# Kernel tuning notes

Measured on AMD Instinct MI355X. Metric: run time of the kernel, lower is better.

## Reference

```python
import jax, jax.numpy as jnp
import numpy as np

HEADS = 8
CH = 256
DH = CH // HEADS  # 32
NB = 128          # nb_features
EPS = 1e-4


def setup_inputs() -> dict:
    key = jax.random.key(0)
    ks = jax.random.split(key, 8)
    b, c, h, w = 4, CH, 96, 96
    s = 1.0 / np.sqrt(CH)  # typical linear init scale
    x = jax.random.normal(ks[0], (b, c, h, w), dtype=jnp.float32)
    wq = jax.random.normal(ks[1], (CH, CH), dtype=jnp.float32) * s
    wk = jax.random.normal(ks[2], (CH, CH), dtype=jnp.float32) * s
    wv = jax.random.normal(ks[3], (CH, CH), dtype=jnp.float32) * s
    wo = jax.random.normal(ks[4], (CH, CH), dtype=jnp.float32) * s
    bo = jnp.zeros((CH,), dtype=jnp.float32)
    # FAVOR+ gaussian orthogonal random projection (nb_features, dim_head)
    pm = np.random.default_rng(0)
    blocks = []
    for _ in range(NB // DH):
        qmat, _ = np.linalg.qr(pm.standard_normal((DH, DH)))
        blocks.append(qmat.T)
    proj = np.concatenate(blocks, axis=0)
    # scale rows to chi-distributed norms (scaling=0 default in performer_pytorch)
    norms = np.linalg.norm(pm.standard_normal((NB, DH)), axis=1, keepdims=True)
    proj_mat = jnp.asarray(proj * norms, dtype=jnp.float32)
    wp = jax.random.normal(ks[5], (CH, CH, 1, 1), dtype=jnp.float32) * s
    bp = jnp.zeros((CH,), dtype=jnp.float32)
    return {"x": x, "wq": wq, "wk": wk, "wv": wv, "wo": wo, "bo": bo,
            "proj_mat": proj_mat, "wp": wp, "bp": bp}


def softmax_kernel(data, proj, is_query):
    # data: (b, h, n, d); proj: (m, d). Performer FAVOR+ positive softmax features.
    data_normalizer = data.shape[-1] ** -0.25
    ratio = proj.shape[0] ** -0.5
    data_dash = jnp.einsum('bhnd,md->bhnm', data * data_normalizer, proj)
    diag = (jnp.sum(data * data, axis=-1) * 0.5 * (data_normalizer ** 2))[..., None]
    if is_query:
        m = jnp.max(data_dash, axis=-1, keepdims=True)
    else:
        m = jnp.max(data_dash, axis=(-1, -2), keepdims=True)
    return ratio * (jnp.exp(data_dash - diag - m) + EPS)


def reference(x, wq, wk, wv, wo, bo, proj_mat, wp, bp):
    b, c, h, w = x.shape
    n = h * w
    xf = x.reshape(b, c, n).transpose(0, 2, 1)  # (b, n, c)

    def split_heads(t):
        return t.reshape(b, n, HEADS, DH).transpose(0, 2, 1, 3)  # (b, h, n, d)

    q = split_heads(xf @ wq.T)
    k = split_heads(xf @ wk.T)
    v = split_heads(xf @ wv.T)

    qp = softmax_kernel(q, proj_mat, True)   # (b, h, n, m)
    kp = softmax_kernel(k, proj_mat, False)  # (b, h, n, m)

    # non-causal linear attention
    k_sum = jnp.sum(kp, axis=-2)                                   # (b, h, m)
    d_inv = 1.0 / jnp.einsum('bhnm,bhm->bhn', qp, k_sum)           # (b, h, n)
    ctx = jnp.einsum('bhnm,bhnd->bhmd', kp, v)                     # (b, h, m, d)
    out = jnp.einsum('bhnm,bhmd->bhnd', qp, ctx) * d_inv[..., None]

    out = out.transpose(0, 2, 1, 3).reshape(b, n, c)  # merge heads
    out = out @ wo.T + bo                              # to_out (attn_out_bias=True)
    out = out.transpose(0, 2, 1).reshape(b, c, h, w)
    # 1x1 conv projection
    out = jnp.einsum('bchw,oc->bohw', out, wp[:, :, 0, 0]) + bp[None, :, None, None]
    return out
```

## Files before the change

### kernel.cpp

```cpp
#include <hip/hip_runtime.h>

#define NTOT 9216
#define NORMC 0.42044820762685725f
#define RATIO 0.08838834764831845f
#define FEPS 1e-4f

typedef _Float16 h8 __attribute__((ext_vector_type(8)));
typedef _Float16 h4 __attribute__((ext_vector_type(4)));
typedef float f4 __attribute__((ext_vector_type(4)));

__device__ __forceinline__ void gld16(const _Float16* g, _Float16* l) {
  __builtin_amdgcn_global_load_lds((const __attribute__((address_space(1))) void*)g,
                                   (__attribute__((address_space(3))) void*)l, 16, 0, 0);
}

__global__ __launch_bounds__(256) void prep_small(
    const float* __restrict__ wq, const float* __restrict__ wk,
    const float* __restrict__ wv, const float* __restrict__ proj,
    const float* __restrict__ wo, const float* __restrict__ bo,
    const float* __restrict__ wp, const float* __restrict__ bp,
    _Float16* __restrict__ Wall, _Float16* __restrict__ projh,
    _Float16* __restrict__ Wc, float* __restrict__ bc) {
  int r = blockIdx.x, t = threadIdx.x;
  if (r < 768) {
    const float* src = (r < 256) ? wq + (size_t)r * 256
                     : (r < 512) ? wk + (size_t)(r - 256) * 256
                                 : wv + (size_t)(r - 512) * 256;
    Wall[(size_t)r * 256 + t] = (_Float16)src[t];
  } else if (r < 784) {
    int idx = (r - 768) * 256 + t;
    projh[idx] = (_Float16)proj[idx];
  } else {
    int o = r - 784;
    float acc = 0.f;
    for (int c = 0; c < 256; ++c) acc += wp[o * 256 + c] * wo[c * 256 + t];
    Wc[o * 256 + t] = (_Float16)acc;
    if (t == 0) {
      float ab = bp[o];
      for (int c = 0; c < 256; ++c) ab += wp[o * 256 + c] * bo[c];
      bc[o] = ab;
    }
  }
}

__global__ __launch_bounds__(256) void prep_xT(
    const float* __restrict__ x, _Float16* __restrict__ xT) {
  __shared__ float T_s[64][65];
  int n0 = blockIdx.x * 64, c0 = blockIdx.y * 64, b = blockIdx.z;
  int t = threadIdx.x;
  for (int i = 0; i < 4; ++i) {
    int f = t + i * 256;
    int cc = f >> 4, n4 = f & 15;
    float4 a = *(const float4*)(x + ((size_t)(b * 256 + c0 + cc)) * NTOT + n0 + n4 * 4);
    T_s[cc][n4 * 4 + 0] = a.x;
    T_s[cc][n4 * 4 + 1] = a.y;
    T_s[cc][n4 * 4 + 2] = a.z;
    T_s[cc][n4 * 4 + 3] = a.w;
  }
  __syncthreads();
  for (int i = 0; i < 2; ++i) {
    int f = t + i * 256;
    int nn = f >> 3, c8 = f & 7;
    h8 hv;
    for (int j = 0; j < 8; ++j) hv[j] = (_Float16)T_s[c8 * 8 + j][nn];
    *(h8*)(xT + ((size_t)(b * NTOT + n0 + nn)) * 256 + c0 + c8 * 8) = hv;
  }
}

__global__ __launch_bounds__(256) void qkv_mfma(
    const _Float16* __restrict__ xT, const _Float16* __restrict__ Wall,
    _Float16* __restrict__ q, _Float16* __restrict__ k, _Float16* __restrict__ v) {
  __shared__ __align__(16) _Float16 A_s[128 * 32];
  __shared__ __align__(16) _Float16 B_s[128 * 32];
  int n0 = blockIdx.x * 128, co0 = blockIdx.y * 128, sel = blockIdx.z;
  _Float16* Out = (sel == 0) ? q : (sel == 1) ? k : v;
  const _Float16* Wb = Wall + (size_t)sel * 65536;
  int t = threadIdx.x, wave = t >> 6, lane = t & 63;
  int lm = lane & 15, lg = lane >> 4;
  int wm = (wave & 1) * 64, wn = (wave >> 1) * 64;
  int srow = wave * 32 + (lane >> 2);
  int scol = ((lane & 3) ^ ((lane >> 3) & 3)) * 8;
  const _Float16* gA = Wb + (size_t)(co0 + srow) * 256 + scol;
  const _Float16* gB = xT + (size_t)(n0 + srow) * 256 + scol;
  _Float16* lA = A_s + wave * 1024;
  _Float16* lB = B_s + wave * 1024;
  int pg = (lg ^ ((lm >> 1) & 3)) * 8;
  f4 acc[4][4] = {};
  for (int kt = 0; kt < 8; ++kt) {
    int c0 = kt * 32;
    __syncthreads();
    gld16(gA + c0, lA);
    gld16(gA + c0 + 16 * 256, lA + 512);
    gld16(gB + c0, lB);
    gld16(gB + c0 + 16 * 256, lB + 512);
    __syncthreads();
    h8 a[4], bf[4];
#pragma unroll
    for (int mi = 0; mi < 4; ++mi) a[mi] = *(const h8*)&A_s[(wm + mi * 16 + lm) * 32 + pg];
#pragma unroll
    for (int ni = 0; ni < 4; ++ni) bf[ni] = *(const h8*)&B_s[(wn + ni * 16 + lm) * 32 + pg];
#pragma unroll
    for (int mi = 0; mi < 4; ++mi)
#pragma unroll
      for (int ni = 0; ni < 4; ++ni)
        acc[mi][ni] = __builtin_amdgcn_mfma_f32_16x16x32_f16(a[mi], bf[ni], acc[mi][ni], 0, 0, 0);
  }
#pragma unroll
  for (int mi = 0; mi < 4; ++mi)
#pragma unroll
    for (int ni = 0; ni < 4; ++ni) {
      h4 hv;
#pragma unroll
      for (int r = 0; r < 4; ++r) hv[r] = (_Float16)acc[mi][ni][r];
      *(h4*)(Out + (size_t)(n0 + wn + ni * 16 + lm) * 256 + co0 + wm + mi * 16 + lg * 4) = hv;
    }
}

__global__ __launch_bounds__(256) void prep_vT(
    const _Float16* __restrict__ v, _Float16* __restrict__ vT) {
  __shared__ _Float16 T[64 * 132];
  int n0 = blockIdx.x * 128, c0 = blockIdx.y * 64, b = blockIdx.z;
  int t = threadIdx.x;
  for (int i = 0; i < 4; ++i) {
    int f = t + i * 256;
    int nl = f >> 3, cg = f & 7;
    h8 vv = *(const h8*)(v + ((size_t)(b * NTOT + n0 + nl)) * 256 + c0 + cg * 8);
#pragma unroll
    for (int j = 0; j < 8; ++j) T[(cg * 8 + j) * 132 + nl] = vv[j];
  }
  __syncthreads();
  int cl = t >> 2, seg = t & 3;
  _Float16* gout = vT + ((size_t)(b * 256 + c0 + cl)) * NTOT + n0 + seg * 32;
#pragma unroll
  for (int j = 0; j < 8; ++j)
    *(h4*)(gout + j * 4) = *(const h4*)&T[cl * 132 + seg * 32 + j * 4];
}

__global__ __launch_bounds__(256) void kmax_mfma(
    const _Float16* __restrict__ k, const _Float16* __restrict__ projh,
    float* __restrict__ kmaxp) {
  __shared__ __align__(16) _Float16 k_s[128 * 32];
  __shared__ float red4[4];
  int bh = blockIdx.y, b = bh >> 3, h = bh & 7;
  int nbase = blockIdx.x * 256;
  int t = threadIdx.x, wave = t >> 6, lane = t & 63, lm = lane & 15, lg = lane >> 4;
  h8 pr[8];
#pragma unroll
  for (int mt = 0; mt < 8; ++mt) pr[mt] = *(const h8*)&projh[(mt * 16 + lm) * 32 + lg * 8];
  int scol = ((lane & 3) ^ ((lane >> 3) & 3)) * 8;
  const _Float16* gK =
      k + ((size_t)(b * NTOT + nbase + wave * 32 + (lane >> 2))) * 256 + h * 32 + scol;
  _Float16* lK = k_s + wave * 1024;
  int pg = (lg ^ ((lm >> 1) & 3)) * 8;
  float vmax = -1e30f;
  for (int ch = 0; ch < 2; ++ch) {
    __syncthreads();
    gld16(gK + (size_t)(ch * 128) * 256, lK);
    gld16(gK + (size_t)(ch * 128) * 256 + 16 * 256, lK + 512);
    __syncthreads();
#pragma unroll
    for (int nt = 0; nt < 2; ++nt) {
      h8 a = *(const h8*)&k_s[(wave * 32 + nt * 16 + lm) * 32 + pg];
#pragma unroll
      for (int mt = 0; mt < 8; ++mt) {
        f4 z = {0.f, 0.f, 0.f, 0.f};
        f4 d = __builtin_amdgcn_mfma_f32_16x16x32_f16(a, pr[mt], z, 0, 0, 0);
        vmax = fmaxf(vmax, fmaxf(fmaxf(d[0], d[1]), fmaxf(d[2], d[3])));
      }
    }
  }
  for (int i = 1; i < 64; i <<= 1) vmax = fmaxf(vmax, __shfl_xor(vmax, i, 64));
  if (lane == 0) red4[wave] = vmax;
  __syncthreads();
  if (t == 0)
    kmaxp[bh * 36 + blockIdx.x] =
        NORMC * fmaxf(fmaxf(red4[0], red4[1]), fmaxf(red4[2], red4[3]));
}

__global__ __launch_bounds__(256) void ctx_mfma(
    const _Float16* __restrict__ k, const _Float16* __restrict__ vT,
    const _Float16* __restrict__ projh, const float* __restrict__ kmaxp,
    float* __restrict__ part) {
  __shared__ __align__(16) _Float16 k_s[128 * 32];
  __shared__ __align__(16) _Float16 vT_s[32 * 136];
  __shared__ __align__(16) _Float16 kpT[128 * 136];
  __shared__ float diag_s[128];
  __shared__ float kmax_sh;
  int bh = blockIdx.y, b = bh >> 3, h = bh & 7;
  int nbase = blockIdx.x * 384;
  int t = threadIdx.x, wave = t >> 6, lane = t & 63, lm = lane & 15, lg = lane >> 4;
  h8 pr[8];
#pragma unroll
  for (int mt = 0; mt < 8; ++mt) pr[mt] = *(const h8*)&projh[(mt * 16 + lm) * 32 + lg * 8];
  if (t == 0) {
    float mx = -1e30f;
    for (int i = 0; i < 36; ++i) mx = fmaxf(mx, kmaxp[bh * 36 + i]);
    kmax_sh = mx;
  }
  __syncthreads();
  float kmax = kmax_sh;
  int scol = ((lane & 3) ^ ((lane >> 3) & 3)) * 8;
  const _Float16* gK =
      k + ((size_t)(b * NTOT + nbase + wave * 32 + (lane >> 2))) * 256 + h * 32 + scol;
  const _Float16* gV = vT + ((size_t)(b * 256 + h * 32 + (t >> 3))) * NTOT + nbase;
  _Float16* lK = k_s + wave * 1024;
  int pg = (lg ^ ((lm >> 1) & 3)) * 8;
  f4 cacc[2][2] = {};
  float ks[8] = {};
  for (int ch = 0; ch < 3; ++ch) {
    gld16(gK + (size_t)(ch * 128) * 256, lK);
    gld16(gK + (size_t)(ch * 128) * 256 + 16 * 256, lK + 512);
    {
      int d = t >> 3, g = t & 7;
#pragma unroll
      for (int i = 0; i < 2; ++i) {
        h8 vv = *(const h8*)(gV + ch * 128 + (i * 8 + g) * 8);
        *(h8*)&vT_s[d * 136 + (i * 8 + g) * 8] = vv;
      }
    }
    __syncthreads();
    if (t < 128) {
      float s = 0.f;
#pragma unroll
      for (int c = 0; c < 4; ++c) {
        h8 kv = *(const h8*)&k_s[t * 32 + c * 8];
#pragma unroll
        for (int j = 0; j < 8; ++j) s += (float)kv[j] * (float)kv[j];
      }
      diag_s[t] = s * (0.5f * NORMC * NORMC);
    }
    f4 dsh[2][8];
#pragma unroll
    for (int nt = 0; nt < 2; ++nt) {
      h8 a = *(const h8*)&k_s[(wave * 32 + nt * 16 + lm) * 32 + pg];
#pragma unroll
      for (int mt = 0; mt < 8; ++mt) {
        f4 z = {0.f, 0.f, 0.f, 0.f};
        dsh[nt][mt] = __builtin_amdgcn_mfma_f32_16x16x32_f16(a, pr[mt], z, 0, 0, 0);
      }
    }
    __syncthreads();
#pragma unroll
    for (int nt = 0; nt < 2; ++nt)
#pragma unroll
      for (int mt = 0; mt < 8; ++mt) {
        h4 hv;
        float lsum = 0.f;
#pragma unroll
        for (int r = 0; r < 4; ++r) {
          int nl = wave * 32 + nt * 16 + lg * 4 + r;
          float val = RATIO * (__expf(NORMC * dsh[nt][mt][r] - diag_s[nl] - kmax) + FEPS);
          hv[r] = (_Float16)val;
          lsum += val;
        }
        ks[mt] += lsum;
        *(h4*)&kpT[(mt * 16 + lm) * 136 + wave * 32 + nt * 16 + lg * 4] = hv;
      }
    __syncthreads();
#pragma unroll
    for (int k2 = 0; k2 < 4; ++k2) {
      h8 a2[2], b2[2];
#pragma unroll
      for (int mt2 = 0; mt2 < 2; ++mt2)
        a2[mt2] = *(const h8*)&kpT[(wave * 32 + mt2 * 16 + lm) * 136 + k2 * 32 + lg * 8];
#pragma unroll
      for (int dt = 0; dt < 2; ++dt)
        b2[dt] = *(const h8*)&vT_s[(dt * 16 + lm) * 136 + k2 * 32 + lg * 8];
#pragma unroll
      for (int mt2 = 0; mt2 < 2; ++mt2)
#pragma unroll
        for (int dt = 0; dt < 2; ++dt)
          cacc[mt2][dt] =
              __builtin_amdgcn_mfma_f32_16x16x32_f16(a2[mt2], b2[dt], cacc[mt2][dt], 0, 0, 0);
    }
    __syncthreads();
  }
  float* pp = part + (size_t)(blockIdx.y * 24 + blockIdx.x) * 4224;
#pragma unroll
  for (int mt2 = 0; mt2 < 2; ++mt2)
#pragma unroll
    for (int dt = 0; dt < 2; ++dt)
      *(f4*)(pp + (dt * 16 + lm) * 128 + wave * 32 + mt2 * 16 + lg * 4) = cacc[mt2][dt];
  float* redk = (float*)kpT;
#pragma unroll
  for (int mt = 0; mt < 8; ++mt) {
    float s = ks[mt];
    s += __shfl_xor(s, 16, 64);
    s += __shfl_xor(s, 32, 64);
    if (lg == 0) redk[wave * 128 + mt * 16 + lm] = s;
  }
  __syncthreads();
  if (t < 128)
    pp[32 * 128 + t] = redk[t] + redk[128 + t] + redk[256 + t] + redk[384 + t];
}

__global__ __launch_bounds__(256) void reduce_ctx(
    const float* __restrict__ part, float* __restrict__ ctx_aug) {
  int bh = blockIdx.x, t = threadIdx.x;
  const float* pb = part + (size_t)bh * 24 * 4224;
  for (int it = 0; it < 17; ++it) {
    int cell = t + it * 256;
    if (cell < 4224) {
      float s = 0.f;
      for (int p = 0; p < 24; ++p) s += pb[(size_t)p * 4224 + cell];
      int d = cell >> 7, m = cell & 127;
      ctx_aug[(size_t)bh * 4608 + m * 36 + d] = s;
    }
  }
}

__global__ __launch_bounds__(256) void attn_mfma(
    const _Float16* __restrict__ q, const _Float16* __restrict__ projh,
    const float* __restrict__ ctx_aug, _Float16* __restrict__ attn) {
  __shared__ __align__(16) _Float16 q_sh[128 * 32];
  __shared__ __align__(16) _Float16 qp_s[128 * 136];
  __shared__ __align__(16) _Float16 ctxT[32 * 136];
  __shared__ float ksum_s[128];
  int n0 = blockIdx.x * 128;
  int bh = blockIdx.y, b = bh >> 3, h = bh & 7;
  int t = threadIdx.x, wave = t >> 6, lane = t & 63, lm = lane & 15, lg = lane >> 4;
  const float* cb = ctx_aug + (size_t)bh * 4608;
  h8 pr[8];
#pragma unroll
  for (int mt = 0; mt < 8; ++mt) pr[mt] = *(const h8*)&projh[(mt * 16 + lm) * 32 + lg * 8];
  int scol = ((lane & 3) ^ ((lane >> 3) & 3)) * 8;
  const _Float16* gQ =
      q + ((size_t)(b * NTOT + n0 + wave * 32 + (lane >> 2))) * 256 + h * 32 + scol;
  gld16(gQ, q_sh + wave * 1024);
  gld16(gQ + 16 * 256, q_sh + wave * 1024 + 512);
  {
    int m = t >> 1, dbase = (t & 1) * 16;
#pragma unroll
    for (int g = 0; g < 4; ++g) {
      float4 cv = *(const float4*)(cb + m * 36 + dbase + g * 4);
      ctxT[(dbase + g * 4 + 0) * 136 + m] = (_Float16)cv.x;
      ctxT[(dbase + g * 4 + 1) * 136 + m] = (_Float16)cv.y;
      ctxT[(dbase + g * 4 + 2) * 136 + m] = (_Float16)cv.z;
      ctxT[(dbase + g * 4 + 3) * 136 + m] = (_Float16)cv.w;
    }
  }
  if (t < 128) ksum_s[t] = cb[t * 36 + 32];
  __syncthreads();
  int pg = (lg ^ ((lm >> 1) & 3)) * 8;
  float diag_r[2];
#pragma unroll
  for (int nt = 0; nt < 2; ++nt) {
    int n = wave * 32 + nt * 16 + lm;
    float s = 0.f;
#pragma unroll
    for (int c = 0; c < 4; ++c) {
      h8 qv = *(const h8*)&q_sh[n * 32 + c * 8];
#pragma unroll
      for (int j = 0; j < 8; ++j) s += (float)qv[j] * (float)qv[j];
    }
    diag_r[nt] = s * (0.5f * NORMC * NORMC);
  }
  f4 dsh[2][8];
#pragma unroll
  for (int nt = 0; nt < 2; ++nt) {
    h8 qf = *(const h8*)&q_sh[(wave * 32 + nt * 16 + lm) * 32 + pg];
#pragma unroll
    for (int mt = 0; mt < 8; ++mt) {
      f4 z = {0.f, 0.f, 0.f, 0.f};
      dsh[nt][mt] = __builtin_amdgcn_mfma_f32_16x16x32_f16(pr[mt], qf, z, 0, 0, 0);
    }
  }
  float den_r[2];
#pragma unroll
  for (int nt = 0; nt < 2; ++nt) {
    float mx = -1e30f;
#pragma unroll
    for (int mt = 0; mt < 8; ++mt)
#pragma unroll
      for (int r = 0; r < 4; ++r) mx = fmaxf(mx, dsh[nt][mt][r]);
    mx = fmaxf(mx, __shfl_xor(mx, 16, 64));
    mx = fmaxf(mx, __shfl_xor(mx, 32, 64));
    float den = 0.f;
#pragma unroll
    for (int mt = 0; mt < 8; ++mt) {
      h4 hv;
#pragma unroll
      for (int r = 0; r < 4; ++r) {
        float val = RATIO * (__expf(NORMC * (dsh[nt][mt][r] - mx) - diag_r[nt]) + FEPS);
        hv[r] = (_Float16)val;
        den += val * ksum_s[mt * 16 + lg * 4 + r];
      }
      *(h4*)&qp_s[(wave * 32 + nt * 16 + lm) * 136 + mt * 16 + lg * 4] = hv;
    }
    den += __shfl_xor(den, 16, 64);
    den += __shfl_xor(den, 32, 64);
    den_r[nt] = 1.f / den;
  }
  __syncthreads();
  f4 oacc[2][2] = {};
#pragma unroll
  for (int k2 = 0; k2 < 4; ++k2) {
    h8 ac[2], bq[2];
#pragma unroll
    for (int dt = 0; dt < 2; ++dt)
      ac[dt] = *(const h8*)&ctxT[(dt * 16 + lm) * 136 + k2 * 32 + lg * 8];
#pragma unroll
    for (int nt = 0; nt < 2; ++nt)
      bq[nt] = *(const h8*)&qp_s[(wave * 32 + nt * 16 + lm) * 136 + k2 * 32 + lg * 8];
#pragma unroll
    for (int dt = 0; dt < 2; ++dt)
#pragma unroll
      for (int nt = 0; nt < 2; ++nt)
        oacc[dt][nt] = __builtin_amdgcn_mfma_f32_16x16x32_f16(ac[dt], bq[nt], oacc[dt][nt], 0, 0, 0);
  }
#pragma unroll
  for (int dt = 0; dt < 2; ++dt)
#pragma unroll
    for (int nt = 0; nt < 2; ++nt) {
      int n = wave * 32 + nt * 16 + lm;
      h4 hv;
#pragma unroll
      for (int r = 0; r < 4; ++r) hv[r] = (_Float16)(oacc[dt][nt][r] * den_r[nt]);
      *(h4*)(attn + ((size_t)(b * NTOT + n0 + n)) * 256 + h * 32 + dt * 16 + lg * 4) = hv;
    }
}

__global__ __launch_bounds__(256) void out_mfma(
    const _Float16* __restrict__ Wc, const _Float16* __restrict__ attn,
    const float* __restrict__ bc, float* __restrict__ out) {
  __shared__ __align__(16) _Float16 A_s[128 * 32];
  __shared__ __align__(16) _Float16 B_s[128 * 32];
  int bx = blockIdx.x;
  int o0 = blockIdx.y * 128;
  int b = bx / 72, nb0 = (bx % 72) * 128;
  int t = threadIdx.x, wave = t >> 6, lane = t & 63;
  int lm = lane & 15, lg = lane >> 4;
  int wm = (wave & 1) * 64, wn = (wave >> 1) * 64;
  int srow = wave * 32 + (lane >> 2);
  int scol = ((lane & 3) ^ ((lane >> 3) & 3)) * 8;
  const _Float16* gA = Wc + (size_t)(o0 + srow) * 256 + scol;
  const _Float16* gB = attn + (size_t)(b * NTOT + nb0 + srow) * 256 + scol;
  _Float16* lA = A_s + wave * 1024;
  _Float16* lB = B_s + wave * 1024;
  int pg = (lg ^ ((lm >> 1) & 3)) * 8;
  f4 acc[4][4] = {};
  for (int kt = 0; kt < 8; ++kt) {
    int c0 = kt * 32;
    __syncthreads();
    gld16(gA + c0, lA);
    gld16(gA + c0 + 16 * 256, lA + 512);
    gld16(gB + c0, lB);
    gld16(gB + c0 + 16 * 256, lB + 512);
    __syncthreads();
    h8 a[4], bf[4];
#pragma unroll
    for (int mi = 0; mi < 4; ++mi) a[mi] = *(const h8*)&A_s[(wm + mi * 16 + lm) * 32 + pg];
#pragma unroll
    for (int ni = 0; ni < 4; ++ni) bf[ni] = *(const h8*)&B_s[(wn + ni * 16 + lm) * 32 + pg];
#pragma unroll
    for (int mi = 0; mi < 4; ++mi)
#pragma unroll
      for (int ni = 0; ni < 4; ++ni)
        acc[mi][ni] = __builtin_amdgcn_mfma_f32_16x16x32_f16(bf[ni], a[mi], acc[mi][ni], 0, 0, 0);
  }
#pragma unroll
  for (int mi = 0; mi < 4; ++mi) {
    int o = o0 + wm + mi * 16 + lm;
    float bias = bc[o];
#pragma unroll
    for (int ni = 0; ni < 4; ++ni) {
      f4 ov = acc[mi][ni];
      float4 st = make_float4(ov[0] + bias, ov[1] + bias, ov[2] + bias, ov[3] + bias);
      *(float4*)(out + ((size_t)(b * 256 + o)) * NTOT + nb0 + wn + ni * 16 + lg * 4) = st;
    }
  }
}

extern "C" void kernel_launch(void* const* d_in, const int* in_sizes, int n_in,
                              void* d_out, int out_size, void* d_ws, size_t ws_size,
                              hipStream_t stream) {
  const float* x = (const float*)d_in[0];
  const float* wq = (const float*)d_in[1];
  const float* wk = (const float*)d_in[2];
  const float* wv = (const float*)d_in[3];
  const float* wo = (const float*)d_in[4];
  const float* bo = (const float*)d_in[5];
  const float* proj = (const float*)d_in[6];
  const float* wp = (const float*)d_in[7];
  const float* bp = (const float*)d_in[8];
  float* out = (float*)d_out;
  float* ws = (float*)d_ws;

  float* part = ws;
  float* ctx_aug = part + 3244032;
  float* kmaxp = ctx_aug + 147456;
  float* bc = kmaxp + 1152;
  _Float16* hb = (_Float16*)(bc + 256);
  const size_t THALF = (size_t)4 * NTOT * 256;
  _Float16* q_h = hb;
  _Float16* k_h = q_h + THALF;
  _Float16* v_h = k_h + THALF;
  _Float16* xT = v_h + THALF;
  _Float16* vTg = xT + THALF;
  _Float16* Wall = vTg + THALF;
  _Float16* Wc = Wall + 768 * 256;
  _Float16* projh = Wc + 65536;

  prep_small<<<1040, 256, 0, stream>>>(wq, wk, wv, proj, wo, bo, wp, bp, Wall, projh, Wc, bc);
  prep_xT<<<dim3(144, 4, 4), 256, 0, stream>>>(x, xT);
  qkv_mfma<<<dim3(288, 2, 3), 256, 0, stream>>>(xT, Wall, q_h, k_h, v_h);
  prep_vT<<<dim3(72, 4, 4), 256, 0, stream>>>(v_h, vTg);
  kmax_mfma<<<dim3(36, 32), 256, 0, stream>>>(k_h, projh, kmaxp);
  ctx_mfma<<<dim3(24, 32), 256, 0, stream>>>(k_h, vTg, projh, kmaxp, part);
  reduce_ctx<<<32, 256, 0, stream>>>(part, ctx_aug);
  attn_mfma<<<dim3(72, 32), 256, 0, stream>>>(q_h, projh, ctx_aug, xT);
  out_mfma<<<dim3(288, 2), 256, 0, stream>>>(Wc, xT, bc, out);
}
```

Measured before the change: 252.2 us.

## Fuse prep kernels, fold vT transpose and key max into QKV GEMM

Merges prep_small and prep_xT into one launch. The QKV GEMM now writes V directly in transposed layout by swapping the MFMA operands, and it computes the per-tile key-feature max from the K tile held in shared memory, which removes the separate prep_vT and kmax kernels and one full pass over K and V. reduce_ctx is split across four times as many blocks and emits fp16 ctxT plus ksum directly, so attn_mfma loads ctx straight into registers instead of transposing it in shared memory. The cost is extra shared memory and epilogue work in the QKV kernel, with only the K blocks doing the max pass.

```diff
diff --git a/kernel.cpp b/kernel.cpp
--- a/kernel.cpp
+++ b/kernel.cpp
@@ -14,24 +14,50 @@
                                    (__attribute__((address_space(3))) void*)l, 16, 0, 0);
 }
 
-__global__ __launch_bounds__(256) void prep_small(
-    const float* __restrict__ wq, const float* __restrict__ wk,
-    const float* __restrict__ wv, const float* __restrict__ proj,
-    const float* __restrict__ wo, const float* __restrict__ bo,
-    const float* __restrict__ wp, const float* __restrict__ bp,
+__global__ __launch_bounds__(256) void prep(
+    const float* __restrict__ x, const float* __restrict__ wq,
+    const float* __restrict__ wk, const float* __restrict__ wv,
+    const float* __restrict__ proj, const float* __restrict__ wo,
+    const float* __restrict__ bo, const float* __restrict__ wp,
+    const float* __restrict__ bp, _Float16* __restrict__ xT,
     _Float16* __restrict__ Wall, _Float16* __restrict__ projh,
     _Float16* __restrict__ Wc, float* __restrict__ bc) {
+  __shared__ float T_s[64][65];
   int r = blockIdx.x, t = threadIdx.x;
-  if (r < 768) {
-    const float* src = (r < 256) ? wq + (size_t)r * 256
-                     : (r < 512) ? wk + (size_t)(r - 256) * 256
-                                 : wv + (size_t)(r - 512) * 256;
-    Wall[(size_t)r * 256 + t] = (_Float16)src[t];
-  } else if (r < 784) {
-    int idx = (r - 768) * 256 + t;
+  if (r < 2304) {
+    int nx = r % 144, rem = r / 144;
+    int cy = rem & 3, b = rem >> 2;
+    int n0 = nx * 64, c0 = cy * 64;
+    for (int i = 0; i < 4; ++i) {
+      int f = t + i * 256;
+      int cc = f >> 4, n4 = f & 15;
+      float4 a = *(const float4*)(x + ((size_t)(b * 256 + c0 + cc)) * NTOT + n0 + n4 * 4);
+      T_s[cc][n4 * 4 + 0] = a.x;
+      T_s[cc][n4 * 4 + 1] = a.y;
+      T_s[cc][n4 * 4 + 2] = a.z;
+      T_s[cc][n4 * 4 + 3] = a.w;
+    }
+    __syncthreads();
+    for (int i = 0; i < 2; ++i) {
+      int f = t + i * 256;
+      int nn = f >> 3, c8 = f & 7;
+      h8 hv;
+      for (int j = 0; j < 8; ++j) hv[j] = (_Float16)T_s[c8 * 8 + j][nn];
+      *(h8*)(xT + ((size_t)(b * NTOT + n0 + nn)) * 256 + c0 + c8 * 8) = hv;
+    }
+    return;
+  }
+  int r2 = r - 2304;
+  if (r2 < 768) {
+    const float* src = (r2 < 256) ? wq + (size_t)r2 * 256
+                     : (r2 < 512) ? wk + (size_t)(r2 - 256) * 256
+                                  : wv + (size_t)(r2 - 512) * 256;
+    Wall[(size_t)r2 * 256 + t] = (_Float16)src[t];
+  } else if (r2 < 784) {
+    int idx = (r2 - 768) * 256 + t;
     projh[idx] = (_Float16)proj[idx];
   } else {
-    int o = r - 784;
+    int o = r2 - 784;
     float acc = 0.f;
     for (int c = 0; c < 256; ++c) acc += wp[o * 256 + c] * wo[c * 256 + t];
     Wc[o * 256 + t] = (_Float16)acc;
@@ -43,37 +69,17 @@
   }
 }
 
-__global__ __launch_bounds__(256) void prep_xT(
-    const float* __restrict__ x, _Float16* __restrict__ xT) {
-  __shared__ float T_s[64][65];
-  int n0 = blockIdx.x * 64, c0 = blockIdx.y * 64, b = blockIdx.z;
-  int t = threadIdx.x;
-  for (int i = 0; i < 4; ++i) {
-    int f = t + i * 256;
-    int cc = f >> 4, n4 = f & 15;
-    float4 a = *(const float4*)(x + ((size_t)(b * 256 + c0 + cc)) * NTOT + n0 + n4 * 4);
-    T_s[cc][n4 * 4 + 0] = a.x;
-    T_s[cc][n4 * 4 + 1] = a.y;
-    T_s[cc][n4 * 4 + 2] = a.z;
-    T_s[cc][n4 * 4 + 3] = a.w;
-  }
-  __syncthreads();
-  for (int i = 0; i < 2; ++i) {
-    int f = t + i * 256;
-    int nn = f >> 3, c8 = f & 7;
-    h8 hv;
-    for (int j = 0; j < 8; ++j) hv[j] = (_Float16)T_s[c8 * 8 + j][nn];
-    *(h8*)(xT + ((size_t)(b * NTOT + n0 + nn)) * 256 + c0 + c8 * 8) = hv;
-  }
-}
-
 __global__ __launch_bounds__(256) void qkv_mfma(
     const _Float16* __restrict__ xT, const _Float16* __restrict__ Wall,
-    _Float16* __restrict__ q, _Float16* __restrict__ k, _Float16* __restrict__ v) {
+    const _Float16* __restrict__ projh, _Float16* __restrict__ q,
+    _Float16* __restrict__ k, _Float16* __restrict__ vT,
+    float* __restrict__ kmaxp) {
   __shared__ __align__(16) _Float16 A_s[128 * 32];
   __shared__ __align__(16) _Float16 B_s[128 * 32];
-  int n0 = blockIdx.x * 128, co0 = blockIdx.y * 128, sel = blockIdx.z;
-  _Float16* Out = (sel == 0) ? q : (sel == 1) ? k : v;
+  __shared__ __align__(16) _Float16 ktile[64 * 132];
+  int bx = blockIdx.x, co0 = blockIdx.y * 128, sel = blockIdx.z;
+  int b = bx / 72, ntile = bx % 72;
+  int n0 = bx * 128;
   const _Float16* Wb = Wall + (size_t)sel * 65536;
   int t = threadIdx.x, wave = t >> 6, lane = t & 63;
   int lm = lane & 15, lg = lane >> 4;
@@ -86,95 +92,104 @@
   _Float16* lB = B_s + wave * 1024;
   int pg = (lg ^ ((lm >> 1) & 3)) * 8;
   f4 acc[4][4] = {};
-  for (int kt = 0; kt < 8; ++kt) {
-    int c0 = kt * 32;
-    __syncthreads();
-    gld16(gA + c0, lA);
-    gld16(gA + c0 + 16 * 256, lA + 512);
-    gld16(gB + c0, lB);
-    gld16(gB + c0 + 16 * 256, lB + 512);
-    __syncthreads();
-    h8 a[4], bf[4];
-#pragma unroll
-    for (int mi = 0; mi < 4; ++mi) a[mi] = *(const h8*)&A_s[(wm + mi * 16 + lm) * 32 + pg];
-#pragma unroll
-    for (int ni = 0; ni < 4; ++ni) bf[ni] = *(const h8*)&B_s[(wn + ni * 16 + lm) * 32 + pg];
+  if (sel < 2) {
+    for (int kt = 0; kt < 8; ++kt) {
+      int c0 = kt * 32;
+      __syncthreads();
+      gld16(gA + c0, lA);
+      gld16(gA + c0 + 16 * 256, lA + 512);
+      gld16(gB + c0, lB);
+      gld16(gB + c0 + 16 * 256, lB + 512);
+      __syncthreads();
+      h8 a[4], bf[4];
+#pragma unroll
+      for (int mi = 0; mi < 4; ++mi) a[mi] = *(const h8*)&A_s[(wm + mi * 16 + lm) * 32 + pg];
+#pragma unroll
+      for (int ni = 0; ni < 4; ++ni) bf[ni] = *(const h8*)&B_s[(wn + ni * 16 + lm) * 32 + pg];
+#pragma unroll
+      for (int mi = 0; mi < 4; ++mi)
+#pragma unroll
+        for (int ni = 0; ni < 4; ++ni)
+          acc[mi][ni] = __builtin_amdgcn_mfma_f32_16x16x32_f16(a[mi], bf[ni], acc[mi][ni], 0, 0, 0);
+    }
+    _Float16* Out = (sel == 0) ? q : k;
 #pragma unroll
     for (int mi = 0; mi < 4; ++mi)
 #pragma unroll
-      for (int ni = 0; ni < 4; ++ni)
-        acc[mi][ni] = __builtin_amdgcn_mfma_f32_16x16x32_f16(a[mi], bf[ni], acc[mi][ni], 0, 0, 0);
-  }
-#pragma unroll
-  for (int mi = 0; mi < 4; ++mi)
-#pragma unroll
-    for (int ni = 0; ni < 4; ++ni) {
-      h4 hv;
-#pragma unroll
-      for (int r = 0; r < 4; ++r) hv[r] = (_Float16)acc[mi][ni][r];
-      *(h4*)(Out + (size_t)(n0 + wn + ni * 16 + lm) * 256 + co0 + wm + mi * 16 + lg * 4) = hv;
-    }
-}
-
-__global__ __launch_bounds__(256) void prep_vT(
-    const _Float16* __restrict__ v, _Float16* __restrict__ vT) {
-  __shared__ _Float16 T[64 * 132];
-  int n0 = blockIdx.x * 128, c0 = blockIdx.y * 64, b = blockIdx.z;
-  int t = threadIdx.x;
-  for (int i = 0; i < 4; ++i) {
-    int f = t + i * 256;
-    int nl = f >> 3, cg = f & 7;
-    h8 vv = *(const h8*)(v + ((size_t)(b * NTOT + n0 + nl)) * 256 + c0 + cg * 8);
-#pragma unroll
-    for (int j = 0; j < 8; ++j) T[(cg * 8 + j) * 132 + nl] = vv[j];
-  }
-  __syncthreads();
-  int cl = t >> 2, seg = t & 3;
-  _Float16* gout = vT + ((size_t)(b * 256 + c0 + cl)) * NTOT + n0 + seg * 32;
-#pragma unroll
-  for (int j = 0; j < 8; ++j)
-    *(h4*)(gout + j * 4) = *(const h4*)&T[cl * 132 + seg * 32 + j * 4];
-}
-
-__global__ __launch_bounds__(256) void kmax_mfma(
-    const _Float16* __restrict__ k, const _Float16* __restrict__ projh,
-    float* __restrict__ kmaxp) {
-  __shared__ __align__(16) _Float16 k_s[128 * 32];
-  __shared__ float red4[4];
-  int bh = blockIdx.y, b = bh >> 3, h = bh & 7;
-  int nbase = blockIdx.x * 256;
-  int t = threadIdx.x, wave = t >> 6, lane = t & 63, lm = lane & 15, lg = lane >> 4;
-  h8 pr[8];
-#pragma unroll
-  for (int mt = 0; mt < 8; ++mt) pr[mt] = *(const h8*)&projh[(mt * 16 + lm) * 32 + lg * 8];
-  int scol = ((lane & 3) ^ ((lane >> 3) & 3)) * 8;
-  const _Float16* gK =
-      k + ((size_t)(b * NTOT + nbase + wave * 32 + (lane >> 2))) * 256 + h * 32 + scol;
-  _Float16* lK = k_s + wave * 1024;
-  int pg = (lg ^ ((lm >> 1) & 3)) * 8;
-  float vmax = -1e30f;
-  for (int ch = 0; ch < 2; ++ch) {
-    __syncthreads();
-    gld16(gK + (size_t)(ch * 128) * 256, lK);
-    gld16(gK + (size_t)(ch * 128) * 256 + 16 * 256, lK + 512);
-    __syncthreads();
-#pragma unroll
-    for (int nt = 0; nt < 2; ++nt) {
-      h8 a = *(const h8*)&k_s[(wave * 32 + nt * 16 + lm) * 32 + pg];
-#pragma unroll
-      for (int mt = 0; mt < 8; ++mt) {
-        f4 z = {0.f, 0.f, 0.f, 0.f};
-        f4 d = __builtin_amdgcn_mfma_f32_16x16x32_f16(a, pr[mt], z, 0, 0, 0);
-        vmax = fmaxf(vmax, fmaxf(fmaxf(d[0], d[1]), fmaxf(d[2], d[3])));
-      }
-    }
-  }
-  for (int i = 1; i < 64; i <<= 1) vmax = fmaxf(vmax, __shfl_xor(vmax, i, 64));
-  if (lane == 0) red4[wave] = vmax;
-  __syncthreads();
-  if (t == 0)
-    kmaxp[bh * 36 + blockIdx.x] =
-        NORMC * fmaxf(fmaxf(red4[0], red4[1]), fmaxf(red4[2], red4[3]));
+      for (int ni = 0; ni < 4; ++ni) {
+        h4 hv;
+#pragma unroll
+        for (int r = 0; r < 4; ++r) hv[r] = (_Float16)acc[mi][ni][r];
+        *(h4*)(Out + (size_t)(n0 + wn + ni * 16 + lm) * 256 + co0 + wm + mi * 16 + lg * 4) = hv;
+      }
+    if (sel == 1) {
+      h8 pr[8];
+#pragma unroll
+      for (int mt = 0; mt < 8; ++mt)
+        pr[mt] = *(const h8*)&projh[(mt * 16 + lm) * 32 + lg * 8];
+      float vmax = -1e30f;
+      for (int half = 0; half < 2; ++half) {
+        __syncthreads();
+        if ((wave >> 1) == half) {
+#pragma unroll
+          for (int mi = 0; mi < 4; ++mi)
+#pragma unroll
+            for (int ni = 0; ni < 4; ++ni) {
+              h4 hv;
+#pragma unroll
+              for (int r = 0; r < 4; ++r) hv[r] = (_Float16)acc[mi][ni][r];
+              *(h4*)&ktile[(ni * 16 + lm) * 132 + wm + mi * 16 + lg * 4] = hv;
+            }
+        }
+        __syncthreads();
+#pragma unroll
+        for (int nt2 = 0; nt2 < 4; ++nt2) {
+          h8 a = *(const h8*)&ktile[(nt2 * 16 + lm) * 132 + wave * 32 + lg * 8];
+#pragma unroll
+          for (int mt = 0; mt < 8; ++mt) {
+            f4 z = {0.f, 0.f, 0.f, 0.f};
+            f4 d = __builtin_amdgcn_mfma_f32_16x16x32_f16(a, pr[mt], z, 0, 0, 0);
+            vmax = fmaxf(vmax, fmaxf(fmaxf(d[0], d[1]), fmaxf(d[2], d[3])));
+          }
+        }
+      }
+      for (int i = 1; i < 64; i <<= 1) vmax = fmaxf(vmax, __shfl_xor(vmax, i, 64));
+      if (lane == 0) {
+        int h = (co0 >> 5) + wave;
+        kmaxp[(size_t)(b * 8 + h) * 72 + ntile] = NORMC * vmax;
+      }
+    }
+  } else {
+    for (int kt = 0; kt < 8; ++kt) {
+      int c0 = kt * 32;
+      __syncthreads();
+      gld16(gA + c0, lA);
+      gld16(gA + c0 + 16 * 256, lA + 512);
+      gld16(gB + c0, lB);
+      gld16(gB + c0 + 16 * 256, lB + 512);
+      __syncthreads();
+      h8 a[4], bf[4];
+#pragma unroll
+      for (int mi = 0; mi < 4; ++mi) a[mi] = *(const h8*)&A_s[(wm + mi * 16 + lm) * 32 + pg];
+#pragma unroll
+      for (int ni = 0; ni < 4; ++ni) bf[ni] = *(const h8*)&B_s[(wn + ni * 16 + lm) * 32 + pg];
+#pragma unroll
+      for (int mi = 0; mi < 4; ++mi)
+#pragma unroll
+        for (int ni = 0; ni < 4; ++ni)
+          acc[mi][ni] = __builtin_amdgcn_mfma_f32_16x16x32_f16(bf[ni], a[mi], acc[mi][ni], 0, 0, 0);
+    }
+#pragma unroll
+    for (int mi = 0; mi < 4; ++mi)
+#pragma unroll
+      for (int ni = 0; ni < 4; ++ni) {
+        h4 hv;
+#pragma unroll
+        for (int r = 0; r < 4; ++r) hv[r] = (_Float16)acc[mi][ni][r];
+        *(h4*)(vT + ((size_t)(b * 256 + co0 + wm + mi * 16 + lm)) * NTOT +
+               ntile * 128 + wn + ni * 16 + lg * 4) = hv;
+      }
+  }
 }
 
 __global__ __launch_bounds__(256) void ctx_mfma(
@@ -192,12 +207,17 @@
   h8 pr[8];
 #pragma unroll
   for (int mt = 0; mt < 8; ++mt) pr[mt] = *(const h8*)&projh[(mt * 16 + lm) * 32 + lg * 8];
-  if (t == 0) {
-    float mx = -1e30f;
-    for (int i = 0; i < 36; ++i) mx = fmaxf(mx, kmaxp[bh * 36 + i]);
-    kmax_sh = mx;
-  }
-  __syncthreads();
+  {
+    float* kred = (float*)kpT;
+    if (t < 72) kred[t] = kmaxp[(size_t)bh * 72 + t];
+    __syncthreads();
+    if (t == 0) {
+      float mx = -1e30f;
+      for (int i = 0; i < 72; ++i) mx = fmaxf(mx, kred[i]);
+      kmax_sh = mx;
+    }
+    __syncthreads();
+  }
   float kmax = kmax_sh;
   int scol = ((lane & 3) ^ ((lane >> 3) & 3)) * 8;
   const _Float16* gK =
@@ -213,10 +233,8 @@
     {
       int d = t >> 3, g = t & 7;
 #pragma unroll
-      for (int i = 0; i < 2; ++i) {
-        h8 vv = *(const h8*)(gV + ch * 128 + (i * 8 + g) * 8);
-        *(h8*)&vT_s[d * 136 + (i * 8 + g) * 8] = vv;
-      }
+      for (int i = 0; i < 2; ++i)
+        *(h8*)&vT_s[d * 136 + (i * 8 + g) * 8] = *(const h8*)(gV + ch * 128 + (i * 8 + g) * 8);
     }
     __syncthreads();
     if (t < 128) {
@@ -295,31 +313,34 @@
 }
 
 __global__ __launch_bounds__(256) void reduce_ctx(
-    const float* __restrict__ part, float* __restrict__ ctx_aug) {
-  int bh = blockIdx.x, t = threadIdx.x;
+    const float* __restrict__ part, _Float16* __restrict__ ctxT_g,
+    float* __restrict__ ksum_g) {
+  int bh = blockIdx.x >> 2, qtr = blockIdx.x & 3;
+  int t = threadIdx.x;
   const float* pb = part + (size_t)bh * 24 * 4224;
-  for (int it = 0; it < 17; ++it) {
-    int cell = t + it * 256;
-    if (cell < 4224) {
+  for (int it = 0; it < 5; ++it) {
+    int lc = it * 256 + t;
+    if (lc < 1056) {
+      int cell = qtr * 1056 + lc;
       float s = 0.f;
       for (int p = 0; p < 24; ++p) s += pb[(size_t)p * 4224 + cell];
       int d = cell >> 7, m = cell & 127;
-      ctx_aug[(size_t)bh * 4608 + m * 36 + d] = s;
+      if (d < 32) ctxT_g[(size_t)bh * 4096 + d * 128 + m] = (_Float16)s;
+      else ksum_g[(size_t)bh * 128 + m] = s;
     }
   }
 }
 
 __global__ __launch_bounds__(256) void attn_mfma(
     const _Float16* __restrict__ q, const _Float16* __restrict__ projh,
-    const float* __restrict__ ctx_aug, _Float16* __restrict__ attn) {
+    const _Float16* __restrict__ ctxT_g, const float* __restrict__ ksum_g,
+    _Float16* __restrict__ attn) {
   __shared__ __align__(16) _Float16 q_sh[128 * 32];
   __shared__ __align__(16) _Float16 qp_s[128 * 136];
-  __shared__ __align__(16) _Float16 ctxT[32 * 136];
   __shared__ float ksum_s[128];
   int n0 = blockIdx.x * 128;
   int bh = blockIdx.y, b = bh >> 3, h = bh & 7;
   int t = threadIdx.x, wave = t >> 6, lane = t & 63, lm = lane & 15, lg = lane >> 4;
-  const float* cb = ctx_aug + (size_t)bh * 4608;
   h8 pr[8];
 #pragma unroll
   for (int mt = 0; mt < 8; ++mt) pr[mt] = *(const h8*)&projh[(mt * 16 + lm) * 32 + lg * 8];
@@ -328,18 +349,13 @@
       q + ((size_t)(b * NTOT + n0 + wave * 32 + (lane >> 2))) * 256 + h * 32 + scol;
   gld16(gQ, q_sh + wave * 1024);
   gld16(gQ + 16 * 256, q_sh + wave * 1024 + 512);
-  {
-    int m = t >> 1, dbase = (t & 1) * 16;
-#pragma unroll
-    for (int g = 0; g < 4; ++g) {
-      float4 cv = *(const float4*)(cb + m * 36 + dbase + g * 4);
-      ctxT[(dbase + g * 4 + 0) * 136 + m] = (_Float16)cv.x;
-      ctxT[(dbase + g * 4 + 1) * 136 + m] = (_Float16)cv.y;
-      ctxT[(dbase + g * 4 + 2) * 136 + m] = (_Float16)cv.z;
-      ctxT[(dbase + g * 4 + 3) * 136 + m] = (_Float16)cv.w;
-    }
-  }
-  if (t < 128) ksum_s[t] = cb[t * 36 + 32];
+  h8 ac[2][4];
+#pragma unroll
+  for (int dt = 0; dt < 2; ++dt)
+#pragma unroll
+    for (int k2 = 0; k2 < 4; ++k2)
+      ac[dt][k2] = *(const h8*)&ctxT_g[(size_t)bh * 4096 + (dt * 16 + lm) * 128 + k2 * 32 + lg * 8];
+  if (t < 128) ksum_s[t] = ksum_g[(size_t)bh * 128 + t];
   __syncthreads();
   int pg = (lg ^ ((lm >> 1) & 3)) * 8;
   float diag_r[2];
@@ -395,10 +411,7 @@
   f4 oacc[2][2] = {};
 #pragma unroll
   for (int k2 = 0; k2 < 4; ++k2) {
-    h8 ac[2], bq[2];
-#pragma unroll
-    for (int dt = 0; dt < 2; ++dt)
-      ac[dt] = *(const h8*)&ctxT[(dt * 16 + lm) * 136 + k2 * 32 + lg * 8];
+    h8 bq[2];
 #pragma unroll
     for (int nt = 0; nt < 2; ++nt)
       bq[nt] = *(const h8*)&qp_s[(wave * 32 + nt * 16 + lm) * 136 + k2 * 32 + lg * 8];
@@ -406,7 +419,7 @@
     for (int dt = 0; dt < 2; ++dt)
 #pragma unroll
       for (int nt = 0; nt < 2; ++nt)
-        oacc[dt][nt] = __builtin_amdgcn_mfma_f32_16x16x32_f16(ac[dt], bq[nt], oacc[dt][nt], 0, 0, 0);
+        oacc[dt][nt] = __builtin_amdgcn_mfma_f32_16x16x32_f16(ac[dt][k2], bq[nt], oacc[dt][nt], 0, 0, 0);
   }
 #pragma unroll
   for (int dt = 0; dt < 2; ++dt)
@@ -487,27 +500,25 @@
   float* ws = (float*)d_ws;
 
   float* part = ws;
-  float* ctx_aug = part + 3244032;
-  float* kmaxp = ctx_aug + 147456;
-  float* bc = kmaxp + 1152;
+  float* kmaxp = part + 3244032;
+  float* ksum_g = kmaxp + 2304;
+  float* bc = ksum_g + 4096;
   _Float16* hb = (_Float16*)(bc + 256);
   const size_t THALF = (size_t)4 * NTOT * 256;
   _Float16* q_h = hb;
   _Float16* k_h = q_h + THALF;
-  _Float16* v_h = k_h + THALF;
-  _Float16* xT = v_h + THALF;
+  _Float16* xT = k_h + THALF;
   _Float16* vTg = xT + THALF;
   _Float16* Wall = vTg + THALF;
   _Float16* Wc = Wall + 768 * 256;
   _Float16* projh = Wc + 65536;
-
-  prep_small<<<1040, 256, 0, stream>>>(wq, wk, wv, proj, wo, bo, wp, bp, Wall, projh, Wc, bc);
-  prep_xT<<<dim3(144, 4, 4), 256, 0, stream>>>(x, xT);
-  qkv_mfma<<<dim3(288, 2, 3), 256, 0, stream>>>(xT, Wall, q_h, k_h, v_h);
-  prep_vT<<<dim3(72, 4, 4), 256, 0, stream>>>(v_h, vTg);
-  kmax_mfma<<<dim3(36, 32), 256, 0, stream>>>(k_h, projh, kmaxp);
+  _Float16* ctxT_g = projh + 4096;
+
+  prep<<<3344, 256, 0, stream>>>(x, wq, wk, wv, proj, wo, bo, wp, bp,
+                                 xT, Wall, projh, Wc, bc);
+  qkv_mfma<<<dim3(288, 2, 3), 256, 0, stream>>>(xT, Wall, projh, q_h, k_h, vTg, kmaxp);
   ctx_mfma<<<dim3(24, 32), 256, 0, stream>>>(k_h, vTg, projh, kmaxp, part);
-  reduce_ctx<<<32, 256, 0, stream>>>(part, ctx_aug);
-  attn_mfma<<<dim3(72, 32), 256, 0, stream>>>(q_h, projh, ctx_aug, xT);
+  reduce_ctx<<<128, 256, 0, stream>>>(part, ctxT_g, ksum_g);
+  attn_mfma<<<dim3(72, 32), 256, 0, stream>>>(q_h, projh, ctxT_g, ksum_g, xT);
   out_mfma<<<dim3(288, 2), 256, 0, stream>>>(Wc, xT, bc, out);
 }
```

After: 222.4 us. -11.8%, faster.
